# Kernel optimization log

Hardware: AMD Instinct MI355X
Metric: run time of the kernel (lower is better)

Reference implementation:

```python
import jax, jax.numpy as jnp
import numpy as np

NEG_INF = -jnp.inf


def setup_inputs() -> dict:
    B, T, D = 2, 512, 256
    key = jax.random.key(0)
    ks = jax.random.split(key, 12)
    inp = {
        'x': jax.random.normal(ks[0], (B, T, D), jnp.float32),
        'last_x': jnp.zeros((B, 1, D), jnp.float32),
        'last_num': jnp.zeros((B, 1, D), jnp.float32),
        'last_den': jnp.zeros((B, 1, D), jnp.float32),
        'time_decay': jax.random.normal(ks[1], (D,), jnp.float32) * 0.5,
        'time_first': jax.random.normal(ks[2], (D,), jnp.float32) * 0.5,
        'time_mix_k': jax.random.uniform(ks[3], (1, 1, D), jnp.float32),
        'time_mix_v': jax.random.uniform(ks[4], (1, 1, D), jnp.float32),
        'time_mix_r': jax.random.uniform(ks[5], (1, 1, D), jnp.float32),
        'Wk': jax.random.normal(ks[6], (D, D), jnp.float32) * 0.02,
        'Wv': jax.random.normal(ks[7], (D, D), jnp.float32) * 0.02,
        'Wr': jax.random.normal(ks[8], (D, D), jnp.float32) * 0.02,
        'Wo': jax.random.normal(ks[9], (D, D), jnp.float32) * 0.02,
    }
    return inp


def reference(x, last_x, last_num, last_den, time_decay, time_first,
              time_mix_k, time_mix_v, time_mix_r, Wk, Wv, Wr, Wo):
    B, T, D = x.shape

    # time_shift: prepend last_x, drop last step
    xs = jnp.concatenate([last_x, x[:, :-1, :]], axis=1)  # (B,T,D)

    k = (x * time_mix_k + xs * (1.0 - time_mix_k)) @ Wk.T
    v = (x * time_mix_v + xs * (1.0 - time_mix_v)) @ Wv.T
    r = (x * time_mix_r + xs * (1.0 - time_mix_r)) @ Wr.T
    sr = jax.nn.sigmoid(r)

    # --- run_wkv (quadratic exp-masked formulation, faithful to source) ---
    w = -jnp.exp(time_decay)                      # (D,)
    t = jnp.arange(T + 1, dtype=x.dtype)
    # wt[i, j] = j - i
    wt = t[None, :T] - t[:T, None]                # (T,T)
    tw = w[None, :] * t[1:, None]                 # (T,D): w * (j+1)
    twt = w[None, None, :] * wt[:, :, None]       # (T,T,D)
    # causal mask: -inf where j < i (strictly lower triangle, tril_(-1))
    ii = jnp.arange(T)
    mask = jnp.where(ii[:, None] > ii[None, :], NEG_INF, 0.0).astype(x.dtype)
    ktw = twt[None] + k[:, :, None, :] + mask[None, :, :, None]  # (B,T,T,D)
    etw = jnp.exp(tw)                             # (T,D)
    ektw = jnp.exp(ktw)                           # (B,T,T,D)
    num = etw[None] * last_num + jnp.einsum('bijd,bid->bjd', ektw, v)  # (B,T,D)
    den = etw[None] * last_den + ektw.sum(axis=1)                      # (B,T,D)
    num_prev = jnp.concatenate([last_num, num[:, :-1, :]], axis=1)
    den_prev = jnp.concatenate([last_den, den[:, :-1, :]], axis=1)
    euk = jnp.exp(time_first[None, None, :] + k)
    wkv = (num_prev + euk * v) / (den_prev + euk)
    # ----------------------------------------------------------------------

    out = (wkv * sr) @ Wo.T
    return (out, x[:, -1:, :], num[:, -1:, :], den[:, -1:, :])
```

## Files before the change

kernel.cpp:

```cpp
#include <hip/hip_runtime.h>

#define TT 512
#define DD 256
#define BB 2
#define MM (BB*TT)
#define LCH 16

__global__ __launch_bounds__(256)
void gemm_mix_t(const float* __restrict__ X, const float* __restrict__ Xlast,
                const float* __restrict__ W0, const float* __restrict__ W1,
                const float* __restrict__ W2,
                const float* __restrict__ mx0, const float* __restrict__ mx1,
                const float* __restrict__ mx2,
                float* __restrict__ O0, float* __restrict__ O1,
                float* __restrict__ O2)
{
    const int mat = blockIdx.z;
    const float* W  = (mat == 0) ? W0  : (mat == 1) ? W1  : W2;
    const float* mx = (mat == 0) ? mx0 : (mat == 1) ? mx1 : mx2;
    float*       O  = (mat == 0) ? O0  : (mat == 1) ? O1  : O2;

    const int n0  = blockIdx.x * 32;
    const int m0  = blockIdx.y * 32;
    const int b   = m0 >> 9;
    const int t0  = m0 & (TT - 1);
    const int tid = threadIdx.x;

    const int tm = tid >> 5;
    const int tn = tid & 31;

    __shared__ float As[32][68];
    __shared__ float Bs[32][68];

    const int rowS[2] = { tid >> 4, (tid + 256) >> 4 };
    const int c4S[2]  = { (tid & 15) * 4, (tid & 15) * 4 };

    float4 aR[2][2], wR[2][2];

    auto load_chunk = [&](int k0, float4 aO[2], float4 wO[2]) {
        #pragma unroll
        for (int p = 0; p < 2; ++p) {
            const int row = rowS[p], c4 = c4S[p];
            const float4 xc = *(const float4*)&X[(m0 + row) * DD + k0 + c4];
            float4 xp;
            if (t0 + row == 0) xp = *(const float4*)&Xlast[b * DD + k0 + c4];
            else               xp = *(const float4*)&X[(m0 + row - 1) * DD + k0 + c4];
            const float4 mv = *(const float4*)&mx[k0 + c4];
            aO[p].x = xp.x + (xc.x - xp.x) * mv.x;
            aO[p].y = xp.y + (xc.y - xp.y) * mv.y;
            aO[p].z = xp.z + (xc.z - xp.z) * mv.z;
            aO[p].w = xp.w + (xc.w - xp.w) * mv.w;
            wO[p] = *(const float4*)&W[(n0 + row) * DD + k0 + c4];
        }
    };

    float acc[4] = {0.f, 0.f, 0.f, 0.f};

    load_chunk(0, aR[0], wR[0]);

    for (int c = 0; c < 4; ++c) {
        const int cur = c & 1;
        #pragma unroll
        for (int p = 0; p < 2; ++p) {
            *(float4*)&As[rowS[p]][c4S[p]] = aR[cur][p];
            *(float4*)&Bs[rowS[p]][c4S[p]] = wR[cur][p];
        }
        __syncthreads();
        if (c < 3) load_chunk(64 * (c + 1), aR[cur ^ 1], wR[cur ^ 1]);
        #pragma unroll
        for (int k4 = 0; k4 < 16; ++k4) {
            const float4 bq = *(const float4*)&Bs[tn][k4 * 4];
            #pragma unroll
            for (int i = 0; i < 4; ++i) {
                const float4 aq = *(const float4*)&As[tm * 4 + i][k4 * 4];
                acc[i] = fmaf(aq.x, bq.x, acc[i]);
                acc[i] = fmaf(aq.y, bq.y, acc[i]);
                acc[i] = fmaf(aq.z, bq.z, acc[i]);
                acc[i] = fmaf(aq.w, bq.w, acc[i]);
            }
        }
        __syncthreads();
    }

    *(float4*)&O[(size_t)(b * DD + n0 + tn) * TT + t0 + tm * 4] =
        make_float4(acc[0], acc[1], acc[2], acc[3]);
}

__global__ __launch_bounds__(256)
void wkv_scan(const float* __restrict__ kT, const float* __restrict__ vT,
              const float* __restrict__ rT, const float* __restrict__ x,
              const float* __restrict__ last_num, const float* __restrict__ last_den,
              const float* __restrict__ time_decay, const float* __restrict__ time_first,
              float* __restrict__ yT, float* __restrict__ out)
{
    const int tid  = threadIdx.x;
    const int ch   = blockIdx.x * 8 + (tid >> 5);
    const int lane = tid & 31;
    const int b    = ch >> 8;
    const int d    = ch & (DD - 1);

    const float w  = -__expf(time_decay[d]);
    const float ew = __expf(w);
    const float eu = __expf(time_first[d]);

    const size_t base = (size_t)ch * TT + lane * LCH;
    float k_[LCH], v_[LCH], r_[LCH];
    #pragma unroll
    for (int i = 0; i < 4; ++i) {
        *(float4*)&k_[4 * i] = *(const float4*)(kT + base + 4 * i);
        *(float4*)&v_[4 * i] = *(const float4*)(vT + base + 4 * i);
        *(float4*)&r_[4 * i] = *(const float4*)(rT + base + 4 * i);
    }

    float ek[LCH], ekv[LCH], sr[LCH];
    #pragma unroll
    for (int i = 0; i < LCH; ++i) {
        ek[i]  = __expf(k_[i]);
        ekv[i] = ek[i] * v_[i];
        sr[i]  = __builtin_amdgcn_rcpf(1.0f + __expf(-r_[i]));
    }

    float A = __expf(w * (float)LCH);
    float Bn = 0.0f, Bd = 0.0f;
    #pragma unroll
    for (int i = 0; i < LCH; ++i) {
        Bn = fmaf(ew, Bn, ekv[i]);
        Bd = fmaf(ew, Bd, ek[i]);
    }

    #pragma unroll
    for (int s = 1; s < 32; s <<= 1) {
        const float Ax  = __shfl_up(A, s, 32);
        const float Bnx = __shfl_up(Bn, s, 32);
        const float Bdx = __shfl_up(Bd, s, 32);
        if (lane >= s) {
            Bn = fmaf(A, Bnx, Bn);
            Bd = fmaf(A, Bdx, Bd);
            A *= Ax;
        }
    }

    float Aex  = __shfl_up(A, 1, 32);
    float Bnex = __shfl_up(Bn, 1, 32);
    float Bdex = __shfl_up(Bd, 1, 32);
    if (lane == 0) { Aex = 1.0f; Bnex = 0.0f; Bdex = 0.0f; }
    float sn = fmaf(Aex, last_num[ch], Bnex);
    float sd = fmaf(Aex, last_den[ch], Bdex);

    float y_[LCH];
    #pragma unroll
    for (int i = 0; i < LCH; ++i) {
        const float euk = eu * ek[i];
        const float wkv = (sn + eu * ekv[i]) * __builtin_amdgcn_rcpf(sd + euk);
        y_[i] = wkv * sr[i];
        sn = fmaf(ew, sn, ekv[i]);
        sd = fmaf(ew, sd, ek[i]);
    }
    #pragma unroll
    for (int i = 0; i < 4; ++i)
        *(float4*)(yT + base + 4 * i) = *(const float4*)&y_[4 * i];

    if (lane == 31) {
        out[MM * DD + BB * DD + ch]     = sn;
        out[MM * DD + 2 * BB * DD + ch] = sd;
    }
    if (lane == 0)
        out[MM * DD + ch] = x[(b * TT + TT - 1) * DD + d];
}

__global__ __launch_bounds__(256)
void gemm_out(const float* __restrict__ yT, const float* __restrict__ Wo,
              float* __restrict__ O)
{
    const int n0  = blockIdx.x * 32;
    const int m0  = blockIdx.y * 32;
    const int b   = m0 >> 9;
    const int t0  = m0 & (TT - 1);
    const int tid = threadIdx.x;

    const int tm = tid >> 5;
    const int tn = tid & 31;

    __shared__ float As[64][36];
    __shared__ float Bs[32][68];

    const int rowA[2] = { tid >> 3, (tid + 256) >> 3 };
    const int c4A     = (tid & 7) * 4;
    const int rowB[2] = { tid >> 4, (tid + 256) >> 4 };
    const int c4B     = (tid & 15) * 4;

    float4 aR[2][2], wR[2][2];

    auto load_chunk = [&](int k0, float4 aO[2], float4 wO[2]) {
        #pragma unroll
        for (int p = 0; p < 2; ++p) {
            aO[p] = *(const float4*)&yT[(size_t)(b * DD + k0 + rowA[p]) * TT + t0 + c4A];
            wO[p] = *(const float4*)&Wo[(n0 + rowB[p]) * DD + k0 + c4B];
        }
    };

    float acc[4] = {0.f, 0.f, 0.f, 0.f};

    load_chunk(0, aR[0], wR[0]);

    for (int c = 0; c < 4; ++c) {
        const int cur = c & 1;
        #pragma unroll
        for (int p = 0; p < 2; ++p) {
            *(float4*)&As[rowA[p]][c4A] = aR[cur][p];
            *(float4*)&Bs[rowB[p]][c4B] = wR[cur][p];
        }
        __syncthreads();
        if (c < 3) load_chunk(64 * (c + 1), aR[cur ^ 1], wR[cur ^ 1]);
        #pragma unroll
        for (int k4 = 0; k4 < 16; ++k4) {
            const float4 bq = *(const float4*)&Bs[tn][k4 * 4];
            const float bb[4] = {bq.x, bq.y, bq.z, bq.w};
            #pragma unroll
            for (int j = 0; j < 4; ++j) {
                const float4 aq = *(const float4*)&As[k4 * 4 + j][tm * 4];
                acc[0] = fmaf(aq.x, bb[j], acc[0]);
                acc[1] = fmaf(aq.y, bb[j], acc[1]);
                acc[2] = fmaf(aq.z, bb[j], acc[2]);
                acc[3] = fmaf(aq.w, bb[j], acc[3]);
            }
        }
        __syncthreads();
    }

    #pragma unroll
    for (int i = 0; i < 4; ++i)
        O[(size_t)(m0 + tm * 4 + i) * DD + n0 + tn] = acc[i];
}

extern "C" void kernel_launch(void* const* d_in, const int* in_sizes, int n_in,
                              void* d_out, int out_size, void* d_ws, size_t ws_size,
                              hipStream_t stream)
{
    const float* x    = (const float*)d_in[0];
    const float* lx   = (const float*)d_in[1];
    const float* lnum = (const float*)d_in[2];
    const float* lden = (const float*)d_in[3];
    const float* td   = (const float*)d_in[4];
    const float* tf   = (const float*)d_in[5];
    const float* mk   = (const float*)d_in[6];
    const float* mv   = (const float*)d_in[7];
    const float* mr   = (const float*)d_in[8];
    const float* Wk   = (const float*)d_in[9];
    const float* Wv   = (const float*)d_in[10];
    const float* Wr   = (const float*)d_in[11];
    const float* Wo   = (const float*)d_in[12];
    float* out = (float*)d_out;

    float* kT = (float*)d_ws;
    float* vT = kT + MM * DD;
    float* rT = vT + MM * DD;
    float* yT = rT + MM * DD;

    gemm_mix_t<<<dim3(8, 32, 3), 256, 0, stream>>>(
        x, lx, Wk, Wv, Wr, mk, mv, mr, kT, vT, rT);

    wkv_scan<<<dim3(64), 256, 0, stream>>>(
        kT, vT, rT, x, lnum, lden, td, tf, yT, out);

    gemm_out<<<dim3(8, 32), 256, 0, stream>>>(yT, Wo, out);
}
```

Measured before the change: 113.6 us.

## Fuse three RWKV kernels into one persistent kernel with grid barriers

```diff
diff --git a/kernel.cpp b/kernel.cpp
--- a/kernel.cpp
+++ b/kernel.cpp
@@ -5,232 +5,238 @@
 #define BB 2
 #define MM (BB*TT)
 #define LCH 16
+#define NBLK 256
+
+__device__ __forceinline__ void grid_barrier(int* cnt, int* flag)
+{
+    __syncthreads();
+    if (threadIdx.x == 0) {
+        __threadfence();
+        int v = __hip_atomic_fetch_add(cnt, 1, __ATOMIC_ACQ_REL,
+                                       __HIP_MEMORY_SCOPE_AGENT);
+        if (v == NBLK - 1) {
+            __hip_atomic_store(flag, 1, __ATOMIC_RELEASE,
+                               __HIP_MEMORY_SCOPE_AGENT);
+        } else {
+            while (!__hip_atomic_load(flag, __ATOMIC_ACQUIRE,
+                                      __HIP_MEMORY_SCOPE_AGENT))
+                __builtin_amdgcn_s_sleep(4);
+        }
+        __threadfence();
+    }
+    __syncthreads();
+}
 
 __global__ __launch_bounds__(256)
-void gemm_mix_t(const float* __restrict__ X, const float* __restrict__ Xlast,
-                const float* __restrict__ W0, const float* __restrict__ W1,
-                const float* __restrict__ W2,
-                const float* __restrict__ mx0, const float* __restrict__ mx1,
-                const float* __restrict__ mx2,
-                float* __restrict__ O0, float* __restrict__ O1,
-                float* __restrict__ O2)
+void rwkv_fused(const float* __restrict__ x,    const float* __restrict__ xlast,
+                const float* __restrict__ lnum, const float* __restrict__ lden,
+                const float* __restrict__ td,   const float* __restrict__ tf,
+                const float* __restrict__ mk,   const float* __restrict__ mvx,
+                const float* __restrict__ mr,
+                const float* __restrict__ Wk,   const float* __restrict__ Wv,
+                const float* __restrict__ Wr,   const float* __restrict__ Wo,
+                float* __restrict__ kT, float* __restrict__ vT,
+                float* __restrict__ rT, float* __restrict__ yT,
+                float* __restrict__ out, int* __restrict__ bar)
 {
-    const int mat = blockIdx.z;
-    const float* W  = (mat == 0) ? W0  : (mat == 1) ? W1  : W2;
-    const float* mx = (mat == 0) ? mx0 : (mat == 1) ? mx1 : mx2;
-    float*       O  = (mat == 0) ? O0  : (mat == 1) ? O1  : O2;
-
-    const int n0  = blockIdx.x * 32;
-    const int m0  = blockIdx.y * 32;
-    const int b   = m0 >> 9;
-    const int t0  = m0 & (TT - 1);
+    __shared__ union {
+        struct { float A[3][32][64]; float B[3][32][64]; } p1;
+        struct { float A[64][32];    float B[32][64];    } p3;
+    } sm;
+
+    const int bid = blockIdx.x;
     const int tid = threadIdx.x;
 
-    const int tm = tid >> 5;
-    const int tn = tid & 31;
-
-    __shared__ float As[32][68];
-    __shared__ float Bs[32][68];
-
-    const int rowS[2] = { tid >> 4, (tid + 256) >> 4 };
-    const int c4S[2]  = { (tid & 15) * 4, (tid & 15) * 4 };
-
-    float4 aR[2][2], wR[2][2];
-
-    auto load_chunk = [&](int k0, float4 aO[2], float4 wO[2]) {
-        #pragma unroll
-        for (int p = 0; p < 2; ++p) {
-            const int row = rowS[p], c4 = c4S[p];
-            const float4 xc = *(const float4*)&X[(m0 + row) * DD + k0 + c4];
-            float4 xp;
-            if (t0 + row == 0) xp = *(const float4*)&Xlast[b * DD + k0 + c4];
-            else               xp = *(const float4*)&X[(m0 + row - 1) * DD + k0 + c4];
-            const float4 mv = *(const float4*)&mx[k0 + c4];
-            aO[p].x = xp.x + (xc.x - xp.x) * mv.x;
-            aO[p].y = xp.y + (xc.y - xp.y) * mv.y;
-            aO[p].z = xp.z + (xc.z - xp.z) * mv.z;
-            aO[p].w = xp.w + (xc.w - xp.w) * mv.w;
-            wO[p] = *(const float4*)&W[(n0 + row) * DD + k0 + c4];
-        }
-    };
-
-    float acc[4] = {0.f, 0.f, 0.f, 0.f};
-
-    load_chunk(0, aR[0], wR[0]);
-
-    for (int c = 0; c < 4; ++c) {
-        const int cur = c & 1;
-        #pragma unroll
-        for (int p = 0; p < 2; ++p) {
-            *(float4*)&As[rowS[p]][c4S[p]] = aR[cur][p];
-            *(float4*)&Bs[rowS[p]][c4S[p]] = wR[cur][p];
-        }
-        __syncthreads();
-        if (c < 3) load_chunk(64 * (c + 1), aR[cur ^ 1], wR[cur ^ 1]);
-        #pragma unroll
-        for (int k4 = 0; k4 < 16; ++k4) {
-            const float4 bq = *(const float4*)&Bs[tn][k4 * 4];
-            #pragma unroll
-            for (int i = 0; i < 4; ++i) {
-                const float4 aq = *(const float4*)&As[tm * 4 + i][k4 * 4];
-                acc[i] = fmaf(aq.x, bq.x, acc[i]);
-                acc[i] = fmaf(aq.y, bq.y, acc[i]);
-                acc[i] = fmaf(aq.z, bq.z, acc[i]);
-                acc[i] = fmaf(aq.w, bq.w, acc[i]);
-            }
-        }
-        __syncthreads();
-    }
-
-    *(float4*)&O[(size_t)(b * DD + n0 + tn) * TT + t0 + tm * 4] =
-        make_float4(acc[0], acc[1], acc[2], acc[3]);
-}
-
-__global__ __launch_bounds__(256)
-void wkv_scan(const float* __restrict__ kT, const float* __restrict__ vT,
-              const float* __restrict__ rT, const float* __restrict__ x,
-              const float* __restrict__ last_num, const float* __restrict__ last_den,
-              const float* __restrict__ time_decay, const float* __restrict__ time_first,
-              float* __restrict__ yT, float* __restrict__ out)
-{
-    const int tid  = threadIdx.x;
-    const int ch   = blockIdx.x * 8 + (tid >> 5);
-    const int lane = tid & 31;
-    const int b    = ch >> 8;
-    const int d    = ch & (DD - 1);
-
-    const float w  = -__expf(time_decay[d]);
-    const float ew = __expf(w);
-    const float eu = __expf(time_first[d]);
-
-    const size_t base = (size_t)ch * TT + lane * LCH;
-    float k_[LCH], v_[LCH], r_[LCH];
-    #pragma unroll
-    for (int i = 0; i < 4; ++i) {
-        *(float4*)&k_[4 * i] = *(const float4*)(kT + base + 4 * i);
-        *(float4*)&v_[4 * i] = *(const float4*)(vT + base + 4 * i);
-        *(float4*)&r_[4 * i] = *(const float4*)(rT + base + 4 * i);
-    }
-
-    float ek[LCH], ekv[LCH], sr[LCH];
-    #pragma unroll
-    for (int i = 0; i < LCH; ++i) {
-        ek[i]  = __expf(k_[i]);
-        ekv[i] = ek[i] * v_[i];
-        sr[i]  = __builtin_amdgcn_rcpf(1.0f + __expf(-r_[i]));
-    }
-
-    float A = __expf(w * (float)LCH);
-    float Bn = 0.0f, Bd = 0.0f;
-    #pragma unroll
-    for (int i = 0; i < LCH; ++i) {
-        Bn = fmaf(ew, Bn, ekv[i]);
-        Bd = fmaf(ew, Bd, ek[i]);
-    }
-
-    #pragma unroll
-    for (int s = 1; s < 32; s <<= 1) {
-        const float Ax  = __shfl_up(A, s, 32);
-        const float Bnx = __shfl_up(Bn, s, 32);
-        const float Bdx = __shfl_up(Bd, s, 32);
-        if (lane >= s) {
-            Bn = fmaf(A, Bnx, Bn);
-            Bd = fmaf(A, Bdx, Bd);
-            A *= Ax;
-        }
-    }
-
-    float Aex  = __shfl_up(A, 1, 32);
-    float Bnex = __shfl_up(Bn, 1, 32);
-    float Bdex = __shfl_up(Bd, 1, 32);
-    if (lane == 0) { Aex = 1.0f; Bnex = 0.0f; Bdex = 0.0f; }
-    float sn = fmaf(Aex, last_num[ch], Bnex);
-    float sd = fmaf(Aex, last_den[ch], Bdex);
-
-    float y_[LCH];
-    #pragma unroll
-    for (int i = 0; i < LCH; ++i) {
-        const float euk = eu * ek[i];
-        const float wkv = (sn + eu * ekv[i]) * __builtin_amdgcn_rcpf(sd + euk);
-        y_[i] = wkv * sr[i];
-        sn = fmaf(ew, sn, ekv[i]);
-        sd = fmaf(ew, sd, ek[i]);
-    }
-    #pragma unroll
-    for (int i = 0; i < 4; ++i)
-        *(float4*)(yT + base + 4 * i) = *(const float4*)&y_[4 * i];
-
-    if (lane == 31) {
-        out[MM * DD + BB * DD + ch]     = sn;
-        out[MM * DD + 2 * BB * DD + ch] = sd;
-    }
-    if (lane == 0)
-        out[MM * DD + ch] = x[(b * TT + TT - 1) * DD + d];
-}
-
-__global__ __launch_bounds__(256)
-void gemm_out(const float* __restrict__ yT, const float* __restrict__ Wo,
-              float* __restrict__ O)
-{
-    const int n0  = blockIdx.x * 32;
-    const int m0  = blockIdx.y * 32;
-    const int b   = m0 >> 9;
-    const int t0  = m0 & (TT - 1);
-    const int tid = threadIdx.x;
-
-    const int tm = tid >> 5;
-    const int tn = tid & 31;
-
-    __shared__ float As[64][36];
-    __shared__ float Bs[32][68];
-
-    const int rowA[2] = { tid >> 3, (tid + 256) >> 3 };
-    const int c4A     = (tid & 7) * 4;
-    const int rowB[2] = { tid >> 4, (tid + 256) >> 4 };
-    const int c4B     = (tid & 15) * 4;
-
-    float4 aR[2][2], wR[2][2];
-
-    auto load_chunk = [&](int k0, float4 aO[2], float4 wO[2]) {
-        #pragma unroll
-        for (int p = 0; p < 2; ++p) {
-            aO[p] = *(const float4*)&yT[(size_t)(b * DD + k0 + rowA[p]) * TT + t0 + c4A];
-            wO[p] = *(const float4*)&Wo[(n0 + rowB[p]) * DD + k0 + c4B];
-        }
-    };
-
-    float acc[4] = {0.f, 0.f, 0.f, 0.f};
-
-    load_chunk(0, aR[0], wR[0]);
-
-    for (int c = 0; c < 4; ++c) {
-        const int cur = c & 1;
-        #pragma unroll
-        for (int p = 0; p < 2; ++p) {
-            *(float4*)&As[rowA[p]][c4A] = aR[cur][p];
-            *(float4*)&Bs[rowB[p]][c4B] = wR[cur][p];
-        }
-        __syncthreads();
-        if (c < 3) load_chunk(64 * (c + 1), aR[cur ^ 1], wR[cur ^ 1]);
-        #pragma unroll
-        for (int k4 = 0; k4 < 16; ++k4) {
-            const float4 bq = *(const float4*)&Bs[tn][k4 * 4];
-            const float bb[4] = {bq.x, bq.y, bq.z, bq.w};
-            #pragma unroll
-            for (int j = 0; j < 4; ++j) {
-                const float4 aq = *(const float4*)&As[k4 * 4 + j][tm * 4];
-                acc[0] = fmaf(aq.x, bb[j], acc[0]);
-                acc[1] = fmaf(aq.y, bb[j], acc[1]);
-                acc[2] = fmaf(aq.z, bb[j], acc[2]);
-                acc[3] = fmaf(aq.w, bb[j], acc[3]);
-            }
-        }
-        __syncthreads();
-    }
-
-    #pragma unroll
-    for (int i = 0; i < 4; ++i)
-        O[(size_t)(m0 + tm * 4 + i) * DD + n0 + tn] = acc[i];
+    {
+        const float* Wm[3] = { Wk, Wv, Wr };
+        const float* mx[3] = { mk, mvx, mr };
+        float*       Om[3] = { kT, vT, rT };
+
+        const int n0 = (bid & 7) * 32;
+        const int m0 = (bid >> 3) * 32;
+        const int b  = m0 >> 9;
+        const int t0 = m0 & (TT - 1);
+
+        const int row0 = tid >> 4;
+        const int cq   = tid & 15;
+        const int tm   = tid >> 5;
+        const int tn   = tid & 31;
+
+        float4 acc[3] = { {0,0,0,0}, {0,0,0,0}, {0,0,0,0} };
+
+        for (int c = 0; c < 4; ++c) {
+            const int k0 = c * 64;
+            #pragma unroll
+            for (int p = 0; p < 2; ++p) {
+                const int row = row0 + p * 16;
+                const float4 xc = *(const float4*)&x[(m0 + row) * DD + k0 + cq * 4];
+                float4 xp;
+                if (t0 + row == 0) xp = *(const float4*)&xlast[b * DD + k0 + cq * 4];
+                else               xp = *(const float4*)&x[(m0 + row - 1) * DD + k0 + cq * 4];
+                #pragma unroll
+                for (int m = 0; m < 3; ++m) {
+                    const float4 mv = *(const float4*)&mx[m][k0 + cq * 4];
+                    float4 a;
+                    a.x = xp.x + (xc.x - xp.x) * mv.x;
+                    a.y = xp.y + (xc.y - xp.y) * mv.y;
+                    a.z = xp.z + (xc.z - xp.z) * mv.z;
+                    a.w = xp.w + (xc.w - xp.w) * mv.w;
+                    *(float4*)&sm.p1.A[m][row][cq * 4] = a;
+                    const float4 wv = *(const float4*)&Wm[m][(n0 + row) * DD + k0 + cq * 4];
+                    *(float4*)&sm.p1.B[m][row][(cq ^ (row & 15)) * 4] = wv;
+                }
+            }
+            __syncthreads();
+            #pragma unroll
+            for (int k4 = 0; k4 < 16; ++k4) {
+                #pragma unroll
+                for (int m = 0; m < 3; ++m) {
+                    const float4 bq = *(const float4*)&sm.p1.B[m][tn][(k4 ^ (tn & 15)) * 4];
+                    float* ac = (float*)&acc[m];
+                    #pragma unroll
+                    for (int i = 0; i < 4; ++i) {
+                        const float4 aq = *(const float4*)&sm.p1.A[m][tm * 4 + i][k4 * 4];
+                        ac[i] = fmaf(aq.x, bq.x, ac[i]);
+                        ac[i] = fmaf(aq.y, bq.y, ac[i]);
+                        ac[i] = fmaf(aq.z, bq.z, ac[i]);
+                        ac[i] = fmaf(aq.w, bq.w, ac[i]);
+                    }
+                }
+            }
+            __syncthreads();
+        }
+        #pragma unroll
+        for (int m = 0; m < 3; ++m)
+            *(float4*)&Om[m][(size_t)(b * DD + n0 + tn) * TT + t0 + tm * 4] = acc[m];
+    }
+
+    grid_barrier(bar, bar + 1);
+
+    if (bid < 64) {
+        const int ch   = bid * 8 + (tid >> 5);
+        const int lane = tid & 31;
+        const int b    = ch >> 8;
+        const int d    = ch & (DD - 1);
+
+        const float w  = -__expf(td[d]);
+        const float ew = __expf(w);
+        const float eu = __expf(tf[d]);
+
+        const size_t base = (size_t)ch * TT + lane * LCH;
+        float k_[LCH], v_[LCH], r_[LCH];
+        #pragma unroll
+        for (int i = 0; i < 4; ++i) {
+            *(float4*)&k_[4 * i] = *(const float4*)(kT + base + 4 * i);
+            *(float4*)&v_[4 * i] = *(const float4*)(vT + base + 4 * i);
+            *(float4*)&r_[4 * i] = *(const float4*)(rT + base + 4 * i);
+        }
+
+        float ek[LCH], ekv[LCH], sr[LCH];
+        #pragma unroll
+        for (int i = 0; i < LCH; ++i) {
+            ek[i]  = __expf(k_[i]);
+            ekv[i] = ek[i] * v_[i];
+            sr[i]  = __builtin_amdgcn_rcpf(1.0f + __expf(-r_[i]));
+        }
+
+        float A = __expf(w * (float)LCH);
+        float Bn = 0.0f, Bd = 0.0f;
+        #pragma unroll
+        for (int i = 0; i < LCH; ++i) {
+            Bn = fmaf(ew, Bn, ekv[i]);
+            Bd = fmaf(ew, Bd, ek[i]);
+        }
+
+        #pragma unroll
+        for (int s = 1; s < 32; s <<= 1) {
+            const float Ax  = __shfl_up(A, s, 32);
+            const float Bnx = __shfl_up(Bn, s, 32);
+            const float Bdx = __shfl_up(Bd, s, 32);
+            if (lane >= s) {
+                Bn = fmaf(A, Bnx, Bn);
+                Bd = fmaf(A, Bdx, Bd);
+                A *= Ax;
+            }
+        }
+
+        float Aex  = __shfl_up(A, 1, 32);
+        float Bnex = __shfl_up(Bn, 1, 32);
+        float Bdex = __shfl_up(Bd, 1, 32);
+        if (lane == 0) { Aex = 1.0f; Bnex = 0.0f; Bdex = 0.0f; }
+        float sn = fmaf(Aex, lnum[ch], Bnex);
+        float sd = fmaf(Aex, lden[ch], Bdex);
+
+        float y_[LCH];
+        #pragma unroll
+        for (int i = 0; i < LCH; ++i) {
+            const float euk = eu * ek[i];
+            const float wkv = (sn + eu * ekv[i]) * __builtin_amdgcn_rcpf(sd + euk);
+            y_[i] = wkv * sr[i];
+            sn = fmaf(ew, sn, ekv[i]);
+            sd = fmaf(ew, sd, ek[i]);
+        }
+        #pragma unroll
+        for (int i = 0; i < 4; ++i)
+            *(float4*)(yT + base + 4 * i) = *(const float4*)&y_[4 * i];
+
+        if (lane == 31) {
+            out[MM * DD + BB * DD + ch]     = sn;
+            out[MM * DD + 2 * BB * DD + ch] = sd;
+        }
+        if (lane == 0)
+            out[MM * DD + ch] = x[(b * TT + TT - 1) * DD + d];
+    }
+
+    grid_barrier(bar + 2, bar + 3);
+
+    {
+        const int n0 = (bid & 7) * 32;
+        const int m0 = (bid >> 3) * 32;
+        const int b  = m0 >> 9;
+        const int t0 = m0 & (TT - 1);
+
+        const int tm = tid >> 5;
+        const int tn = tid & 31;
+
+        const int rowA = tid >> 3;
+        const int cqA  = tid & 7;
+        const int rowB = tid >> 4;
+        const int cqB  = tid & 15;
+
+        float acc[4] = {0.f, 0.f, 0.f, 0.f};
+
+        for (int c = 0; c < 4; ++c) {
+            const int k0 = c * 64;
+            #pragma unroll
+            for (int p = 0; p < 2; ++p) {
+                const int ra = rowA + p * 32;
+                *(float4*)&sm.p3.A[ra][cqA * 4] =
+                    *(const float4*)&yT[(size_t)(b * DD + k0 + ra) * TT + t0 + cqA * 4];
+                const int rb = rowB + p * 16;
+                *(float4*)&sm.p3.B[rb][(cqB ^ (rb & 15)) * 4] =
+                    *(const float4*)&Wo[(n0 + rb) * DD + k0 + cqB * 4];
+            }
+            __syncthreads();
+            #pragma unroll
+            for (int k4 = 0; k4 < 16; ++k4) {
+                const float4 bq = *(const float4*)&sm.p3.B[tn][(k4 ^ (tn & 15)) * 4];
+                const float bb[4] = {bq.x, bq.y, bq.z, bq.w};
+                #pragma unroll
+                for (int j = 0; j < 4; ++j) {
+                    const float4 aq = *(const float4*)&sm.p3.A[k4 * 4 + j][tm * 4];
+                    acc[0] = fmaf(aq.x, bb[j], acc[0]);
+                    acc[1] = fmaf(aq.y, bb[j], acc[1]);
+                    acc[2] = fmaf(aq.z, bb[j], acc[2]);
+                    acc[3] = fmaf(aq.w, bb[j], acc[3]);
+                }
+            }
+            __syncthreads();
+        }
+
+        #pragma unroll
+        for (int i = 0; i < 4; ++i)
+            out[(size_t)(m0 + tm * 4 + i) * DD + n0 + tn] = acc[i];
+    }
 }
 
 extern "C" void kernel_launch(void* const* d_in, const int* in_sizes, int n_in,
@@ -256,12 +262,11 @@
     float* vT = kT + MM * DD;
     float* rT = vT + MM * DD;
     float* yT = rT + MM * DD;
-
-    gemm_mix_t<<<dim3(8, 32, 3), 256, 0, stream>>>(
-        x, lx, Wk, Wv, Wr, mk, mv, mr, kT, vT, rT);
-
-    wkv_scan<<<dim3(64), 256, 0, stream>>>(
-        kT, vT, rT, x, lnum, lden, td, tf, yT, out);
-
-    gemm_out<<<dim3(8, 32), 256, 0, stream>>>(yT, Wo, out);
+    int*   bar = (int*)(yT + MM * DD);
+
+    hipMemsetAsync(bar, 0, 4 * sizeof(int), stream);
+
+    rwkv_fused<<<dim3(NBLK), 256, 0, stream>>>(
+        x, lx, lnum, lden, td, tf, mk, mv, mr, Wk, Wv, Wr, Wo,
+        kT, vT, rT, yT, out, bar);
 }
```

Measured after the change: 219.2 us. 1.93x slower.
